# Performance work log

Measured on AMD Instinct MI355X. Metric: run time of the kernel, lower is better.

The kernel has to match this reference:

```python
import jax, jax.numpy as jnp
import numpy as np

_SAMPLING_EPS = 1e-5


def setup_inputs() -> dict:
    key = jax.random.key(0)
    k1, k2, k3, k4, k5 = jax.random.split(key, 5)
    B, V = 128, 128000
    logits = jax.random.normal(k1, (B, V), dtype=jnp.float32)
    temperature = jax.random.uniform(k2, (B,), dtype=jnp.float32)  # some rows < eps -> greedy
    top_k = jax.random.randint(k3, (B,), 1, 64, dtype=jnp.int32)   # in [1, 63]
    top_p = jax.random.uniform(k4, (B,), dtype=jnp.float32, minval=0.05, maxval=1.0)
    noise_u = jax.random.uniform(k5, (B, V), dtype=jnp.float32, minval=1e-10, maxval=1.0)
    return {"logits": logits, "temperature": temperature, "top_k": top_k,
            "top_p": top_p, "noise_u": noise_u, "max_num_logprobs": 5}


def _apply_top_k_top_p(logits, k, p):
    # Faithful to vLLM: ascending sort, top-k threshold mask, top-p cumsum mask, scatter back.
    B, V = logits.shape
    order = jnp.argsort(logits, axis=-1)                       # ascending, [B, V]
    logits_sort = jnp.take_along_axis(logits, order, axis=-1)
    neg_inf = jnp.float32(-jnp.inf)
    # top-k: pivot value at position V - k; everything strictly below it -> -inf
    pivot_idx = (V - k.astype(jnp.int32))[:, None]             # [B, 1]
    pivot = jnp.take_along_axis(logits_sort, pivot_idx, axis=-1)
    logits_sort = jnp.where(logits_sort < pivot, neg_inf, logits_sort)
    # top-p: softmax over sorted logits, cumsum, drop prefix with mass <= 1 - p (keep last)
    probs_sort = jax.nn.softmax(logits_sort, axis=-1)
    probs_sum = jnp.cumsum(probs_sort, axis=-1)
    top_p_mask = probs_sum <= (1.0 - p)[:, None]
    top_p_mask = top_p_mask.at[:, -1].set(False)
    logits_sort = jnp.where(top_p_mask, neg_inf, logits_sort)
    # scatter back to original vocab order
    rows = jnp.arange(B)[:, None]
    return jnp.zeros_like(logits).at[rows, order].set(logits_sort)


def reference(logits, temperature, top_k, top_p, noise_u, max_num_logprobs):
    # temperature scaling (temp < eps means greedy; divide by 1.0 instead)
    temp = jnp.where(temperature < _SAMPLING_EPS, 1.0, temperature)
    logits = logits.astype(jnp.float32) / temp[:, None]
    # top-k / top-p filtering
    logits = _apply_top_k_top_p(logits, top_k, top_p)
    # probabilities and sampling
    probs = jax.nn.softmax(logits, axis=-1)
    greedy = jnp.argmax(probs, axis=-1)
    q = -jnp.log(noise_u)                                      # Exp(1) noise (q.exponential_())
    random = jnp.argmax(probs / q, axis=-1)
    sampled = jnp.where(temperature < _SAMPLING_EPS, greedy, random).astype(jnp.int32)
    # top-k logprobs
    logprobs = jax.nn.log_softmax(logits, axis=-1)
    topk_logprobs, topk_indices = jax.lax.top_k(logprobs, max_num_logprobs)
    return sampled, topk_indices.astype(jnp.int32), topk_logprobs
```

## Files before the change

### kernel.cpp

```cpp
#include <hip/hip_runtime.h>
#include <math.h>
#include <stdint.h>

#define BT     256
#define TOPC   64
#define FT     512
#define SLOTS  32
#define CAPC   8192

__device__ __forceinline__ unsigned f2ord(float f) {
    unsigned u = __float_as_uint(f);
    return u ^ ((u & 0x80000000u) ? 0xFFFFFFFFu : 0x80000000u);
}
__device__ __forceinline__ float ord2f(unsigned k) {
    unsigned u = (k & 0x80000000u) ? (k ^ 0x80000000u) : (k ^ 0xFFFFFFFFu);
    return __uint_as_float(u);
}

__device__ unsigned radix_select_compact4(uint2* s_buf, uint2* s_keep,
                                          unsigned (*s_hist)[16], unsigned* p_cnt2,
                                          unsigned n, int tid, int wid)
{
    unsigned prefix = 0u;
    int remaining = TOPC;
    for (int shift = 28; shift >= 0; shift -= 4) {
        if (tid < 64) ((unsigned*)s_hist)[tid] = 0u;
        __syncthreads();
        for (unsigned i = (unsigned)tid; i < n; i += BT) {
            unsigned k = s_buf[i].x;
            bool ing = (shift == 28) || ((k >> (shift + 4)) == (prefix >> (shift + 4)));
            if (ing) atomicAdd(&s_hist[wid][(k >> shift) & 15u], 1u);
        }
        __syncthreads();
        int cum = 0; int b = 0; unsigned hb = 0u;
        for (int bb = 15; bb >= 0; --bb) {
            unsigned h = s_hist[0][bb] + s_hist[1][bb] + s_hist[2][bb] + s_hist[3][bb];
            cum += (int)h;
            if (cum >= remaining) { b = bb; hb = h; break; }
        }
        remaining -= (cum - (int)hb);
        prefix |= ((unsigned)b) << shift;
        __syncthreads();
    }
    if (tid == 0) *p_cnt2 = 0u;
    __syncthreads();
    for (unsigned i = (unsigned)tid; i < n; i += BT) {
        uint2 c = s_buf[i];
        if (c.x > prefix) s_keep[atomicAdd(p_cnt2, 1u)] = c;
    }
    __syncthreads();
    for (unsigned i = (unsigned)tid; i < n; i += BT) {
        uint2 c = s_buf[i];
        if (c.x == prefix) {
            unsigned pos = atomicAdd(p_cnt2, 1u);
            if (pos < TOPC) s_keep[pos] = c;
        }
    }
    __syncthreads();
    return prefix;
}

__global__ __launch_bounds__(64) void row_thresh(
    const float* __restrict__ logits, unsigned* __restrict__ thr,
    unsigned* __restrict__ ovf, int V)
{
    const int r    = blockIdx.x;
    const int lane = threadIdx.x;
    const float* rowp = logits + (size_t)r * (size_t)V;

    unsigned kr[64];
    #pragma unroll
    for (int g = 0; g < 8; ++g) {
        int c0 = g * 512 + lane * 8;
        if (c0 < V) {
            float4 a = *(const float4*)(rowp + c0);
            float4 b = *(const float4*)(rowp + c0 + 4);
            kr[g * 8 + 0] = f2ord(a.x); kr[g * 8 + 1] = f2ord(a.y);
            kr[g * 8 + 2] = f2ord(a.z); kr[g * 8 + 3] = f2ord(a.w);
            kr[g * 8 + 4] = f2ord(b.x); kr[g * 8 + 5] = f2ord(b.y);
            kr[g * 8 + 6] = f2ord(b.z); kr[g * 8 + 7] = f2ord(b.w);
        } else {
            #pragma unroll
            for (int j = 0; j < 8; ++j) kr[g * 8 + j] = 0u;
        }
    }

    unsigned lo = 0u, hi = 0xFFFFu;
    while (lo < hi) {
        unsigned mid = (lo + hi + 1u) >> 1;
        unsigned t = mid << 16;
        int c = 0;
        #pragma unroll
        for (int j = 0; j < 64; ++j) c += __popcll(__ballot(kr[j] >= t));
        if (c >= TOPC) lo = mid; else hi = mid - 1u;
    }
    if (lane == 0) { thr[r] = lo << 16; ovf[r] = 0u; }
}

__global__ __launch_bounds__(BT) void filter_pass(
    const float* __restrict__ logits, const unsigned* __restrict__ thr,
    unsigned* __restrict__ ovf, uint2* __restrict__ surv,
    int B, int V, int tpr, int slots)
{
    const int tid  = threadIdx.x;
    const int wid  = tid >> 6;
    const int lane = tid & 63;
    const unsigned long long ltm = (1ull << lane) - 1ull;
    const int nw = gridDim.x * (BT / 64);
    const int ntiles = B * tpr;

    for (int tw = blockIdx.x * (BT / 64) + wid; tw < ntiles; tw += nw) {
        const int t    = __builtin_amdgcn_readfirstlane(tw);
        const int row  = t / tpr;
        const int tin  = t - row * tpr;
        const int col0 = tin * FT + lane * 8;
        const bool v   = col0 < V;
        const float* rowp = logits + (size_t)row * (size_t)V;

        unsigned k[8];
        if (v) {
            float4 a = *(const float4*)(rowp + col0);
            float4 b = *(const float4*)(rowp + col0 + 4);
            k[0] = f2ord(a.x); k[1] = f2ord(a.y); k[2] = f2ord(a.z); k[3] = f2ord(a.w);
            k[4] = f2ord(b.x); k[5] = f2ord(b.y); k[6] = f2ord(b.z); k[7] = f2ord(b.w);
        } else {
            #pragma unroll
            for (int j = 0; j < 8; ++j) k[j] = 0u;
        }

        const unsigned tr = thr[row];
        uint2* base = surv + (size_t)t * (unsigned)slots;

        unsigned tot = 0u;
        #pragma unroll
        for (int j = 0; j < 8; ++j) {
            bool pa = v && (k[j] >= tr);
            unsigned long long m = __ballot(pa);
            if (pa) {
                unsigned pos = tot + (unsigned)__popcll(m & ltm);
                if (pos < (unsigned)slots)
                    base[pos] = make_uint2(k[j], (unsigned)(col0 + j));
            }
            tot += (unsigned)__popcll(m);
        }
        if (lane < slots && (unsigned)lane >= tot)
            base[lane] = make_uint2(0u, 0u);
        if (lane == 0 && tot > (unsigned)slots)
            atomicOr(&ovf[row], 1u);
    }
}

__global__ __launch_bounds__(BT) void phase2_combined(
    const uint2* __restrict__ surv, const unsigned* __restrict__ ovf,
    const unsigned* __restrict__ thr, const float* __restrict__ logits,
    const float* __restrict__ temperature,
    const int*   __restrict__ top_k,
    const float* __restrict__ top_p,
    const float* __restrict__ noise_u,
    float* __restrict__ out,
    int B, int V, int M, int tpr, int slots)
{
    __shared__ uint2    s_buf[CAPC];
    __shared__ uint2    s_keep[TOPC];
    __shared__ unsigned s_hist[4][16];
    __shared__ unsigned s_cnt, s_cnt2, s_ovf;
    __shared__ float    sval[TOPC], se[TOPC], sq[TOPC];
    __shared__ int      sidx[TOPC];

    const int r   = blockIdx.x;
    const int tid = threadIdx.x;
    const int wid = tid >> 6;

    const int tslots = tpr * slots;
    const bool fb = (ovf[r] != 0u) || (tslots > CAPC);
    unsigned n;

    if (!fb) {
        const uint2* rs = surv + (size_t)r * (unsigned)tslots;
        for (int i = tid; i < tslots; i += BT)
            s_buf[i] = rs[i];
        n = (unsigned)tslots;
        if (n < TOPC) {
            for (unsigned i = n + (unsigned)tid; i < TOPC; i += BT)
                s_buf[i] = make_uint2(0u, 0u);
            n = TOPC;
        }
        __syncthreads();
    } else {
        const float* rowp = logits + (size_t)r * (size_t)V;
        if (tid == 0) { s_cnt = 0u; s_ovf = 0u; }
        __syncthreads();
        unsigned vst = thr[r];
        bool strict = false;
        for (int t = 0; t < V; t += BT * 8) {
            int bs = t + tid * 8;
            bool v = bs < V;
            unsigned kk[8];
            if (v) {
                float4 a = *(const float4*)(rowp + bs);
                float4 b = *(const float4*)(rowp + bs + 4);
                kk[0] = f2ord(a.x); kk[1] = f2ord(a.y); kk[2] = f2ord(a.z); kk[3] = f2ord(a.w);
                kk[4] = f2ord(b.x); kk[5] = f2ord(b.y); kk[6] = f2ord(b.z); kk[7] = f2ord(b.w);
            } else {
                #pragma unroll
                for (int j = 0; j < 8; ++j) kk[j] = 0u;
            }
            unsigned pm = 0u; int np = 0;
            if (v) {
                #pragma unroll
                for (int j = 0; j < 8; ++j) {
                    bool pa = strict ? (kk[j] > vst) : (kk[j] >= vst);
                    if (pa) { pm |= (1u << j); ++np; }
                }
            }
            for (;;) {
                if (np) {
                    unsigned pos = atomicAdd(&s_cnt, (unsigned)np);
                    unsigned rem = 0u; int nr = 0;
                    #pragma unroll
                    for (int j = 0; j < 8; ++j) {
                        if (pm & (1u << j)) {
                            if (pos < CAPC) s_buf[pos] = make_uint2(kk[j], (unsigned)(bs + j));
                            else { rem |= (1u << j); ++nr; }
                            ++pos;
                        }
                    }
                    if (nr) s_ovf = 1u;
                    pm = rem; np = nr;
                }
                __syncthreads();
                unsigned o = s_ovf;
                __syncthreads();
                if (!o) break;
                unsigned nn2 = s_cnt; if (nn2 > CAPC) nn2 = CAPC;
                unsigned v2s = radix_select_compact4(s_buf, s_keep, s_hist, &s_cnt2,
                                                     nn2, tid, wid);
                if (tid < TOPC) s_buf[tid] = s_keep[tid];
                if (tid == 0) { s_cnt = TOPC; s_ovf = 0u; }
                __syncthreads();
                unsigned rem = 0u; int nr = 0;
                #pragma unroll
                for (int j = 0; j < 8; ++j)
                    if ((pm & (1u << j)) && kk[j] > v2s) { rem |= (1u << j); ++nr; }
                pm = rem; np = nr;
                vst = v2s; strict = true;
            }
        }
        n = s_cnt; if (n > CAPC) n = CAPC;
        if (n < TOPC) {
            for (unsigned i = n + (unsigned)tid; i < TOPC; i += BT)
                s_buf[i] = make_uint2(0u, 0u);
            n = TOPC;
            __syncthreads();
        }
    }

    radix_select_compact4(s_buf, s_keep, s_hist, &s_cnt2, n, tid, wid);

    for (int kk = 2; kk <= TOPC; kk <<= 1) {
        for (int j = kk >> 1; j > 0; j >>= 1) {
            if (tid < TOPC / 2) {
                int i0 = ((tid & ~(j - 1)) << 1) | (tid & (j - 1));
                int i1 = i0 | j;
                bool up = ((i0 & kk) == 0);
                uint2 A = s_keep[i0], Bv = s_keep[i1];
                bool gt = (A.x < Bv.x) || (A.x == Bv.x && A.y > Bv.y);
                if (gt == up) { s_keep[i0] = Bv; s_keep[i1] = A; }
            }
            __syncthreads();
        }
    }

    float temp_orig = temperature[r];
    float temp = (temp_orig < 1e-5f) ? 1.0f : temp_orig;

    if (tid < TOPC) {
        unsigned k = s_keep[tid].x;
        int id = (int)s_keep[tid].y;
        sval[tid] = ord2f(k) / temp;
        sidx[tid] = id;
        float u = noise_u[(size_t)r * (size_t)V + id];
        sq[tid] = -logf(u);
    }
    __syncthreads();
    if (tid < TOPC) se[tid] = expf(sval[tid] - sval[0]);
    __syncthreads();

    if (tid == 0) {
        int k = top_k[r];
        if (k < 1) k = 1; if (k > TOPC) k = TOPC;
        float p = top_p[r];

        float pivot = sval[k - 1];
        int m = k;
        while (m < TOPC && sval[m] >= pivot) ++m;

        float sum = 0.f;
        for (int i = 0; i < m; ++i) sum += se[i];

        float thr1 = 1.0f - p;
        float S = 0.f;
        int f = 1;
        for (int i = m - 1; i >= 1; --i) {
            S += se[i] / sum;
            if (S > thr1) { f = i + 1; break; }
        }

        float sum2 = 0.f;
        for (int i = 0; i < f; ++i) sum2 += se[i];

        int greedy = sidx[0];
        float best = -1.f; int bidx = 0x7fffffff;
        for (int i = 0; i < f; ++i) {
            float ratio = (se[i] / sum2) / sq[i];
            if (ratio > best || (ratio == best && sidx[i] < bidx)) {
                best = ratio; bidx = sidx[i];
            }
        }
        int sampled = (temp_orig < 1e-5f) ? greedy : bidx;

        float lse = logf(sum2);
        out[r] = (float)sampled;
        float* oidx = out + B + (size_t)r * M;
        float* olp  = out + B + (size_t)B * M + (size_t)r * M;
        int produced = 0;
        for (int i = 0; i < f && produced < M; ++i, ++produced) {
            oidx[produced] = (float)sidx[i];
            olp[produced]  = (sval[i] - sval[0]) - lse;
        }
        int v = 0;
        while (produced < M) {
            bool used = false;
            for (int i = 0; i < f; ++i) if (sidx[i] == v) { used = true; break; }
            if (!used) { oidx[produced] = (float)v; olp[produced] = -3.0e38f; ++produced; }
            ++v;
        }
    }
}

extern "C" void kernel_launch(void* const* d_in, const int* in_sizes, int n_in,
                              void* d_out, int out_size, void* d_ws, size_t ws_size,
                              hipStream_t stream)
{
    const float* logits      = (const float*)d_in[0];
    const float* temperature = (const float*)d_in[1];
    const int*   top_k       = (const int*)d_in[2];
    const float* top_p       = (const float*)d_in[3];
    const float* noise_u     = (const float*)d_in[4];

    const int B = in_sizes[1];
    const int V = in_sizes[0] / B;
    const int M = (out_size / B - 1) / 2;

    const int tpr = (V + FT - 1) / FT;

    unsigned* thr = (unsigned*)d_ws;
    unsigned* ovf = thr + B;
    size_t off = (((size_t)2 * B * sizeof(unsigned)) + 7) & ~(size_t)7;
    uint2* surv = (uint2*)((char*)d_ws + off);

    int slots = SLOTS;
    if (ws_size > off) {
        size_t avail = (ws_size - off) / ((size_t)B * tpr * sizeof(uint2));
        if (avail < (size_t)slots) slots = (int)avail;
    } else slots = 1;
    if (slots < 1) slots = 1;
    while (slots > 1 && tpr * slots > CAPC) --slots;

    const int ntiles = B * tpr;
    int fblocks = (ntiles + 3) / 4;
    if (fblocks > 2048) fblocks = 2048;

    row_thresh<<<B, 64, 0, stream>>>(logits, thr, ovf, V);
    filter_pass<<<fblocks, BT, 0, stream>>>(logits, thr, ovf, surv,
                                            B, V, tpr, slots);
    phase2_combined<<<B, BT, 0, stream>>>(surv, ovf, thr, logits,
                                          temperature, top_k, top_p, noise_u,
                                          (float*)d_out, B, V, M, tpr, slots);
}
```

Before: 213.4 us.

## Compact surviving candidates per wavefront in phase2 before selection

Instead of copying every slot of the filter pass (including empty zero slots) into shared memory, each wavefront scans its share of the survivor slots, ballot-compacts the entries that pass the row threshold into a private region, then merges the regions by prefix offsets. The smaller candidate set should shrink the work for the later radix select and sampling, and the shared buffer is halved, which may allow more blocks per CU. The cap on slots per tile is removed. If a wavefront region overflows, the block falls back to rescanning the whole row of logits, which adds a path that could be slow.

```diff
diff --git a/kernel.cpp b/kernel.cpp
--- a/kernel.cpp
+++ b/kernel.cpp
@@ -6,7 +6,8 @@
 #define TOPC   64
 #define FT     512
 #define SLOTS  32
-#define CAPC   8192
+#define CAPW2  1024
+#define CAPC   4096
 
 __device__ __forceinline__ unsigned f2ord(float f) {
     unsigned u = __float_as_uint(f);
@@ -150,7 +151,7 @@
     }
 }
 
-__global__ __launch_bounds__(BT) void phase2_combined(
+__global__ __launch_bounds__(BT) void phase2_sample(
     const uint2* __restrict__ surv, const unsigned* __restrict__ ovf,
     const unsigned* __restrict__ thr, const float* __restrict__ logits,
     const float* __restrict__ temperature,
@@ -163,34 +164,85 @@
     __shared__ uint2    s_buf[CAPC];
     __shared__ uint2    s_keep[TOPC];
     __shared__ unsigned s_hist[4][16];
-    __shared__ unsigned s_cnt, s_cnt2, s_ovf;
+    __shared__ unsigned s_wcnt[4];
+    __shared__ unsigned s_cnt, s_cnt2, s_govf;
     __shared__ float    sval[TOPC], se[TOPC], sq[TOPC];
     __shared__ int      sidx[TOPC];
 
-    const int r   = blockIdx.x;
-    const int tid = threadIdx.x;
-    const int wid = tid >> 6;
-
+    const int r    = blockIdx.x;
+    const int tid  = threadIdx.x;
+    const int wid  = tid >> 6;
+    const int lane = tid & 63;
+    const unsigned long long ltm = (1ull << lane) - 1ull;
+
+    const unsigned tr = thr[r];
     const int tslots = tpr * slots;
-    const bool fb = (ovf[r] != 0u) || (tslots > CAPC);
-    unsigned n;
+    bool fb = (ovf[r] != 0u);
+    unsigned n = 0u;
+
+    if (tid == 0) s_govf = 0u;
+    __syncthreads();
 
     if (!fb) {
         const uint2* rs = surv + (size_t)r * (unsigned)tslots;
-        for (int i = tid; i < tslots; i += BT)
-            s_buf[i] = rs[i];
-        n = (unsigned)tslots;
-        if (n < TOPC) {
-            for (unsigned i = n + (unsigned)tid; i < TOPC; i += BT)
-                s_buf[i] = make_uint2(0u, 0u);
-            n = TOPC;
+        const int share = (tslots + 3) / 4;
+        const int start = wid * share;
+        int end = start + share; if (end > tslots) end = tslots;
+        const int span = end - start;
+        uint2* myreg = &s_buf[wid * CAPW2];
+        unsigned cnt = 0u;
+        for (int j = 0; j < span; j += 64) {
+            int i = start + j + lane;
+            bool inb = i < end;
+            uint2 c = inb ? rs[i] : make_uint2(0u, 0u);
+            bool pa = inb && (c.x >= tr) && (c.x != 0u);
+            unsigned long long m = __ballot(pa);
+            if (pa) {
+                unsigned pos = cnt + (unsigned)__popcll(m & ltm);
+                if (pos < CAPW2) myreg[pos] = c;
+            }
+            cnt += (unsigned)__popcll(m);
+        }
+        if (lane == 0) {
+            s_wcnt[wid] = cnt;
+            if (cnt > CAPW2) s_govf = 1u;
         }
         __syncthreads();
-    } else {
+
+        if (s_govf) {
+            fb = true;
+        } else {
+            unsigned c0 = s_wcnt[0], c1 = s_wcnt[1], c2w = s_wcnt[2], c3 = s_wcnt[3];
+            unsigned off = (wid > 0 ? c0 : 0u) + (wid > 1 ? c1 : 0u)
+                         + (wid > 2 ? c2w : 0u);
+            unsigned mycnt = s_wcnt[wid];
+            uint2 rv[CAPW2 / 64];
+            #pragma unroll
+            for (int g = 0; g < CAPW2 / 64; ++g) {
+                unsigned i = (unsigned)(g * 64 + lane);
+                rv[g] = (i < mycnt) ? myreg[i] : make_uint2(0u, 0u);
+            }
+            __syncthreads();
+            #pragma unroll
+            for (int g = 0; g < CAPW2 / 64; ++g) {
+                unsigned i = (unsigned)(g * 64 + lane);
+                if (i < mycnt) s_buf[off + i] = rv[g];
+            }
+            n = c0 + c1 + c2w + c3;
+            if (n < TOPC) {
+                for (unsigned i = n + (unsigned)tid; i < TOPC; i += BT)
+                    s_buf[i] = make_uint2(0u, 0u);
+                n = TOPC;
+            }
+            __syncthreads();
+        }
+    }
+
+    if (fb) {
         const float* rowp = logits + (size_t)r * (size_t)V;
-        if (tid == 0) { s_cnt = 0u; s_ovf = 0u; }
+        if (tid == 0) { s_cnt = 0u; s_govf = 0u; }
         __syncthreads();
-        unsigned vst = thr[r];
+        unsigned vst = tr;
         bool strict = false;
         for (int t = 0; t < V; t += BT * 8) {
             int bs = t + tid * 8;
@@ -225,18 +277,18 @@
                             ++pos;
                         }
                     }
-                    if (nr) s_ovf = 1u;
+                    if (nr) s_govf = 1u;
                     pm = rem; np = nr;
                 }
                 __syncthreads();
-                unsigned o = s_ovf;
+                unsigned o = s_govf;
                 __syncthreads();
                 if (!o) break;
                 unsigned nn2 = s_cnt; if (nn2 > CAPC) nn2 = CAPC;
                 unsigned v2s = radix_select_compact4(s_buf, s_keep, s_hist, &s_cnt2,
                                                      nn2, tid, wid);
                 if (tid < TOPC) s_buf[tid] = s_keep[tid];
-                if (tid == 0) { s_cnt = TOPC; s_ovf = 0u; }
+                if (tid == 0) { s_cnt = TOPC; s_govf = 0u; }
                 __syncthreads();
                 unsigned rem = 0u; int nr = 0;
                 #pragma unroll
@@ -365,7 +417,6 @@
         if (avail < (size_t)slots) slots = (int)avail;
     } else slots = 1;
     if (slots < 1) slots = 1;
-    while (slots > 1 && tpr * slots > CAPC) --slots;
 
     const int ntiles = B * tpr;
     int fblocks = (ntiles + 3) / 4;
@@ -374,7 +425,7 @@
     row_thresh<<<B, 64, 0, stream>>>(logits, thr, ovf, V);
     filter_pass<<<fblocks, BT, 0, stream>>>(logits, thr, ovf, surv,
                                             B, V, tpr, slots);
-    phase2_combined<<<B, BT, 0, stream>>>(surv, ovf, thr, logits,
-                                          temperature, top_k, top_p, noise_u,
-                                          (float*)d_out, B, V, M, tpr, slots);
-}
+    phase2_sample<<<B, BT, 0, stream>>>(surv, ovf, thr, logits,
+                                        temperature, top_k, top_p, noise_u,
+                                        (float*)d_out, B, V, M, tpr, slots);
+}
```

After: 198.0 us. 1.08x faster.
